# Kernel optimization log

Measured on AMD Instinct MI355X. Metric: run time of the kernel, lower is better.

## Reference

```python
import jax, jax.numpy as jnp
import numpy as np

NUM_HEADS = 4
HEAD_DIM = 16  # out_channels // num_heads = 64 // 4
IN_C = 64
OUT_C = 64


def setup_inputs() -> dict:
    key = jax.random.key(0)
    k1, k2, k3 = jax.random.split(key, 3)
    x = jax.random.normal(k1, (2, IN_C, 64, 64), dtype=jnp.float32)
    # nn.Linear(in_channels, 3*out_channels): weight (3*OUT_C, IN_C), bias (3*OUT_C,)
    s = 1.0 / np.sqrt(IN_C)
    qkv_w = jax.random.uniform(k2, (3 * OUT_C, IN_C), minval=-s, maxval=s, dtype=jnp.float32)
    qkv_b = jax.random.uniform(k3, (3 * OUT_C,), minval=-s, maxval=s, dtype=jnp.float32)
    return {"x": x, "qkv_w": qkv_w, "qkv_b": qkv_b}


def reference(x, qkv_w, qkv_b):
    B, C, H, W = x.shape
    N = H * W
    # (B,C,H,W) -> (B,N,C)
    tokens = x.reshape(B, C, N).transpose(0, 2, 1)
    qkv = tokens @ qkv_w.T + qkv_b  # (B,N,3*OUT_C)
    q, k, v = jnp.split(qkv, 3, axis=-1)
    def to_heads(t):
        return t.reshape(B, N, NUM_HEADS, HEAD_DIM).transpose(0, 2, 1, 3)  # (B,h,N,d)
    q, k, v = to_heads(q), to_heads(k), to_heads(v)
    scale = 1.0 / np.sqrt(HEAD_DIM)
    attn = jnp.einsum('bhnd,bhmd->bhnm', q, k) * scale  # (B,h,N,N)
    attn = jax.nn.softmax(attn, axis=-1)
    # dropout is identity in eval mode
    out = jnp.einsum('bhnm,bhmd->bhnd', attn, v)  # (B,h,N,d)
    out = out.transpose(0, 2, 1, 3).reshape(B, N, OUT_C)  # (B,N,outC)
    out = out.transpose(0, 2, 1).reshape(B, OUT_C, H, W)
    return out
```

## Files before the change

### kernel.cpp

```cpp
#include <hip/hip_runtime.h>
#include <hip/hip_bf16.h>


#define NTOK 4096
#define HD   16
#define BH   8
#define KT   128
#define SCH  (KT/16)
#define HALFK 2048
#define NSTAGE (HALFK/KT)

typedef __attribute__((ext_vector_type(4))) short short4v;
typedef __attribute__((ext_vector_type(4))) float float4v;
typedef __attribute__((ext_vector_type(4))) ushort ushort4v;
typedef __attribute__((ext_vector_type(2))) unsigned uint2v;

__device__ __forceinline__ ushort f2bf(float f) {
  unsigned u = __builtin_bit_cast(unsigned, f);
  u += 0x7fffu + ((u >> 16) & 1u);
  return (ushort)(u >> 16);
}

__device__ __forceinline__ float fast_exp2(float x) {
#if __has_builtin(__builtin_amdgcn_exp2f)
  return __builtin_amdgcn_exp2f(x);
#else
  return exp2f(x);
#endif
}

__device__ __forceinline__ short4v pack4_bf16(float a, float b, float c, float d) {
  __hip_bfloat162 lo = __float22bfloat162_rn(make_float2(a, b));
  __hip_bfloat162 hi = __float22bfloat162_rn(make_float2(c, d));
  unsigned ulo, uhi;
  __builtin_memcpy(&ulo, &lo, 4);
  __builtin_memcpy(&uhi, &hi, 4);
  uint2v u = { ulo, uhi };
  return __builtin_bit_cast(short4v, u);
}

#define QB_OFF 0
#define KB_OFF ((size_t)BH*NTOK*HD)
#define VT_OFF (2*(size_t)BH*NTOK*HD)

__global__ __launch_bounds__(192) void qkv_proj(
    const float* __restrict__ x, const float* __restrict__ w,
    const float* __restrict__ bias, ushort* __restrict__ wsu) {
  const int TOK = 8, TILES = 2;
  int blk = blockIdx.x;
  int b   = blk >> 8;
  int n00 = (blk & 255) * (TOK*TILES);
  int o   = threadIdx.x;

  float wr[64];
  const float4* w4 = reinterpret_cast<const float4*>(w + o*64);
  #pragma unroll
  for (int i = 0; i < 16; ++i) {
    float4 tt = w4[i];
    wr[4*i+0]=tt.x; wr[4*i+1]=tt.y; wr[4*i+2]=tt.z; wr[4*i+3]=tt.w;
  }
  float bb = bias[o];

  int part = o >> 6;
  int oo   = o & 63;
  int h    = oo >> 4;
  int dd   = oo & 15;
  int bh   = b*4 + h;
  const float QSCALE = 0.25f * 1.44269504f;

  ushort* Qt = wsu + QB_OFF;
  ushort* Kb = wsu + KB_OFF;
  ushort* Vt = wsu + VT_OFF;

  __shared__ float4 xs4[64][2];
  const float4* x4 = reinterpret_cast<const float4*>(x);

  #pragma unroll 1
  for (int tile = 0; tile < TILES; ++tile) {
    int n0 = n00 + tile*TOK;
    for (int idx = threadIdx.x; idx < 128; idx += 192) {
      int c = idx >> 1, t4 = idx & 1;
      xs4[c][t4] = x4[((size_t)b*64 + c)*(NTOK/4) + (n0 >> 2) + t4];
    }
    __syncthreads();

    #pragma unroll
    for (int t4 = 0; t4 < 2; ++t4) {
      float a[4] = {bb, bb, bb, bb};
      #pragma unroll
      for (int c = 0; c < 64; ++c) {
        float4 xv = xs4[c][t4];
        float wv = wr[c];
        a[0] = fmaf(xv.x, wv, a[0]);
        a[1] = fmaf(xv.y, wv, a[1]);
        a[2] = fmaf(xv.z, wv, a[2]);
        a[3] = fmaf(xv.w, wv, a[3]);
      }
      if (part == 0) {
        ushort4v vv = { f2bf(a[0]*QSCALE), f2bf(a[1]*QSCALE),
                        f2bf(a[2]*QSCALE), f2bf(a[3]*QSCALE) };
        *(ushort4v*)(Qt + ((size_t)bh*HD + dd)*NTOK + n0 + t4*4) = vv;
      } else if (part == 1) {
        #pragma unroll
        for (int j = 0; j < 4; ++j)
          Kb[((size_t)bh*NTOK + n0 + t4*4 + j)*HD + dd] = f2bf(a[j]);
      } else {
        ushort4v vv = { f2bf(a[0]), f2bf(a[1]), f2bf(a[2]), f2bf(a[3]) };
        *(ushort4v*)(Vt + ((size_t)bh*HD + dd)*NTOK + n0 + t4*4) = vv;
      }
    }
    __syncthreads();
  }
}

__global__ __launch_bounds__(256, 4) void attn_mfma(
    const ushort* __restrict__ wsu, float* __restrict__ out) {
  const ushort* Qt = wsu + QB_OFF;
  const ushort* Kb = wsu + KB_OFF;
  const ushort* Vt = wsu + VT_OFF;

  int bh   = blockIdx.x >> 7;
  int qblk = blockIdx.x & 127;
  int tid  = threadIdx.x;
  int wid  = tid >> 6;
  int lane = tid & 63;
  int lr   = lane & 15;
  int g4   = (lane >> 4) << 2;
  int qg   = wid & 1;
  int half = wid >> 1;
  int qbase = qblk*32 + qg*16;

  __shared__ __align__(16) char tiles[2][2][2][4096];
  __shared__ float comb[2][64][5];

  const ushort* Qh = Qt + (size_t)bh*NTOK*HD;
  const ushort* Kh = Kb + (size_t)bh*NTOK*HD + (size_t)half*HALFK*HD;
  const ushort* Vh = Vt + (size_t)bh*HD*NTOK + half*HALFK;

  short4v qf;
  qf[0] = (short)Qh[(size_t)(g4+0)*NTOK + qbase + lr];
  qf[1] = (short)Qh[(size_t)(g4+1)*NTOK + qbase + lr];
  qf[2] = (short)Qh[(size_t)(g4+2)*NTOK + qbase + lr];
  qf[3] = (short)Qh[(size_t)(g4+3)*NTOK + qbase + lr];

  size_t kgoff = (size_t)((lane >> 5)*16 + (lane & 15))*HD + ((lane >> 4) & 1)*8;
  size_t vgoff = (size_t)(lane & 15)*NTOK + (lane >> 4)*8;

  int loff = ((lane >> 5) << 8) + ((lane & 15) << 4) + (((lane >> 4) & 1) << 3);

  const short4v one4 = {(short)0x3F80, (short)0x3F80, (short)0x3F80, (short)0x3F80};

  float4v acc_e = {0.f,0.f,0.f,0.f}, acc_o = {0.f,0.f,0.f,0.f};
  float4v lac_e = {0.f,0.f,0.f,0.f}, lac_o = {0.f,0.f,0.f,0.f};

#define GLL(g, l_) __builtin_amdgcn_global_load_lds(                        \
    (const __attribute__((address_space(1))) unsigned*)(g),                 \
    (__attribute__((address_space(3))) unsigned*)(l_), 16, 0, 0)

#define STAGE(buf, s) do {                                                  \
    if (qg == 0) {                                                          \
      const ushort* gs = Kh + (size_t)(s)*(KT*HD) + kgoff;                  \
      char* lb = &tiles[buf][half][0][0];                                   \
      GLL(gs, lb); GLL(gs+512, lb+1024);                                    \
      GLL(gs+1024, lb+2048); GLL(gs+1536, lb+3072);                         \
    } else {                                                                \
      const ushort* gs = Vh + (size_t)(s)*KT + vgoff;                       \
      char* lb = &tiles[buf][half][1][0];                                   \
      GLL(gs, lb); GLL(gs+32, lb+1024);                                     \
      GLL(gs+64, lb+2048); GLL(gs+96, lb+3072);                             \
    } } while (0)

#define COMPUTE(buf) do {                                                   \
    const char* kb = &tiles[buf][half][0][0];                               \
    const char* vb = &tiles[buf][half][1][0];                               \
    __builtin_amdgcn_s_setprio(1);                                          \
    _Pragma("unroll")                                                       \
    for (int p = 0; p < SCH/2; ++p) {                                       \
      short4v kf_e = *(const short4v*)(kb + p*1024       + loff);           \
      short4v kf_o = *(const short4v*)(kb + p*1024 + 512 + loff);           \
      short4v vf_e = *(const short4v*)(vb + p*1024       + loff);           \
      short4v vf_o = *(const short4v*)(vb + p*1024 + 512 + loff);           \
      float4v zero = {0.f,0.f,0.f,0.f};                                     \
      float4v se = __builtin_amdgcn_mfma_f32_16x16x16bf16_1k(kf_e, qf, zero, 0,0,0); \
      float4v so = __builtin_amdgcn_mfma_f32_16x16x16bf16_1k(kf_o, qf, zero, 0,0,0); \
      float pe0 = fast_exp2(se[0]), pe1 = fast_exp2(se[1]);                 \
      float pe2 = fast_exp2(se[2]), pe3 = fast_exp2(se[3]);                 \
      float po0 = fast_exp2(so[0]), po1 = fast_exp2(so[1]);                 \
      float po2 = fast_exp2(so[2]), po3 = fast_exp2(so[3]);                 \
      short4v pbe = pack4_bf16(pe0, pe1, pe2, pe3);                         \
      short4v pbo = pack4_bf16(po0, po1, po2, po3);                         \
      acc_e = __builtin_amdgcn_mfma_f32_16x16x16bf16_1k(vf_e, pbe, acc_e, 0,0,0); \
      acc_o = __builtin_amdgcn_mfma_f32_16x16x16bf16_1k(vf_o, pbo, acc_o, 0,0,0); \
      lac_e = __builtin_amdgcn_mfma_f32_16x16x16bf16_1k(one4, pbe, lac_e, 0,0,0); \
      lac_o = __builtin_amdgcn_mfma_f32_16x16x16bf16_1k(one4, pbo, lac_o, 0,0,0); \
    }                                                                       \
    __builtin_amdgcn_s_setprio(0);                                          \
    } while (0)

  STAGE(0, 0);
  __syncthreads();

  #pragma unroll 1
  for (int s = 0; s < NSTAGE; s += 2) {
    if (s + 1 < NSTAGE) STAGE(1, s + 1);
    COMPUTE(0);
    __syncthreads();
    if (s + 2 < NSTAGE) STAGE(0, s + 2);
    COMPUTE(1);
    __syncthreads();
  }

  float a0 = acc_e[0] + acc_o[0];
  float a1 = acc_e[1] + acc_o[1];
  float a2 = acc_e[2] + acc_o[2];
  float a3 = acc_e[3] + acc_o[3];
  float ls = lac_e[0] + lac_o[0];

  if (half == 1) {
    comb[qg][lane][0] = a0; comb[qg][lane][1] = a1;
    comb[qg][lane][2] = a2; comb[qg][lane][3] = a3;
    comb[qg][lane][4] = ls;
  }
  __syncthreads();
  if (half == 0) {
    a0 += comb[qg][lane][0]; a1 += comb[qg][lane][1];
    a2 += comb[qg][lane][2]; a3 += comb[qg][lane][3];
    ls += comb[qg][lane][4];
    float inv = 1.0f / ls;
    int b = bh >> 2, h = bh & 3;
    float* ob = out + ((size_t)(b*64 + h*16 + g4)) * NTOK;
    ob[           qbase + lr] = a0 * inv;
    ob[  NTOK   + qbase + lr] = a1 * inv;
    ob[2*NTOK   + qbase + lr] = a2 * inv;
    ob[3*NTOK   + qbase + lr] = a3 * inv;
  }
#undef GLL
#undef STAGE
#undef COMPUTE
}

extern "C" void kernel_launch(void* const* d_in, const int* in_sizes, int n_in,
                              void* d_out, int out_size, void* d_ws, size_t ws_size,
                              hipStream_t stream) {
  const float* x    = (const float*)d_in[0];
  const float* w    = (const float*)d_in[1];
  const float* bias = (const float*)d_in[2];
  float* out  = (float*)d_out;
  ushort* wsu = (ushort*)d_ws;

  qkv_proj <<<512,  192, 0, stream>>>(x, w, bias, wsu);
  attn_mfma<<<1024, 256, 0, stream>>>(wsu, out);
}
```

Measured before the change: 43.23 us.

## Split KV into quarters with 512-thread blocks, VALU row sums, register-tiled projection

The attention kernel now splits the key range four ways (8 waves per block, smaller 64-key stages) rather than two, reusing the tile LDS for the cross-wave reduction. The row-sum MFMAs against a ones vector are replaced by scalar adds plus cross-lane shuffles. The QKV projection drops its LDS staging and computes 16 tokens per thread directly from global loads. This aims for more waves per CU and fewer MFMA instructions, at the cost of more reduction work, more barriers per key, and extra VALU adds.

```diff
diff --git a/kernel.cpp b/kernel.cpp
--- a/kernel.cpp
+++ b/kernel.cpp
@@ -5,10 +5,10 @@
 #define NTOK 4096
 #define HD   16
 #define BH   8
-#define KT   128
+#define KT   64
 #define SCH  (KT/16)
-#define HALFK 2048
-#define NSTAGE (HALFK/KT)
+#define QUART 1024
+#define NSTAGE (QUART/KT)
 
 typedef __attribute__((ext_vector_type(4))) short short4v;
 typedef __attribute__((ext_vector_type(4))) float float4v;
@@ -46,10 +46,10 @@
 __global__ __launch_bounds__(192) void qkv_proj(
     const float* __restrict__ x, const float* __restrict__ w,
     const float* __restrict__ bias, ushort* __restrict__ wsu) {
-  const int TOK = 8, TILES = 2;
+  const int TOK = 16;
   int blk = blockIdx.x;
   int b   = blk >> 8;
-  int n00 = (blk & 255) * (TOK*TILES);
+  int n0  = (blk & 255) * TOK;
   int o   = threadIdx.x;
 
   float wr[64];
@@ -61,6 +61,25 @@
   }
   float bb = bias[o];
 
+  float a[TOK];
+  #pragma unroll
+  for (int j = 0; j < TOK; ++j) a[j] = bb;
+
+  const float* xb = x + ((size_t)b*64)*NTOK + n0;
+  #pragma unroll 4
+  for (int c = 0; c < 64; ++c) {
+    const float4* xc4 = reinterpret_cast<const float4*>(xb + (size_t)c*NTOK);
+    float wv = wr[c];
+    #pragma unroll
+    for (int q4 = 0; q4 < TOK/4; ++q4) {
+      float4 xv = xc4[q4];
+      a[q4*4+0] = fmaf(xv.x, wv, a[q4*4+0]);
+      a[q4*4+1] = fmaf(xv.y, wv, a[q4*4+1]);
+      a[q4*4+2] = fmaf(xv.z, wv, a[q4*4+2]);
+      a[q4*4+3] = fmaf(xv.w, wv, a[q4*4+3]);
+    }
+  }
+
   int part = o >> 6;
   int oo   = o & 63;
   int h    = oo >> 4;
@@ -72,48 +91,28 @@
   ushort* Kb = wsu + KB_OFF;
   ushort* Vt = wsu + VT_OFF;
 
-  __shared__ float4 xs4[64][2];
-  const float4* x4 = reinterpret_cast<const float4*>(x);
-
-  #pragma unroll 1
-  for (int tile = 0; tile < TILES; ++tile) {
-    int n0 = n00 + tile*TOK;
-    for (int idx = threadIdx.x; idx < 128; idx += 192) {
-      int c = idx >> 1, t4 = idx & 1;
-      xs4[c][t4] = x4[((size_t)b*64 + c)*(NTOK/4) + (n0 >> 2) + t4];
-    }
-    __syncthreads();
-
-    #pragma unroll
-    for (int t4 = 0; t4 < 2; ++t4) {
-      float a[4] = {bb, bb, bb, bb};
-      #pragma unroll
-      for (int c = 0; c < 64; ++c) {
-        float4 xv = xs4[c][t4];
-        float wv = wr[c];
-        a[0] = fmaf(xv.x, wv, a[0]);
-        a[1] = fmaf(xv.y, wv, a[1]);
-        a[2] = fmaf(xv.z, wv, a[2]);
-        a[3] = fmaf(xv.w, wv, a[3]);
-      }
-      if (part == 0) {
-        ushort4v vv = { f2bf(a[0]*QSCALE), f2bf(a[1]*QSCALE),
-                        f2bf(a[2]*QSCALE), f2bf(a[3]*QSCALE) };
-        *(ushort4v*)(Qt + ((size_t)bh*HD + dd)*NTOK + n0 + t4*4) = vv;
-      } else if (part == 1) {
-        #pragma unroll
-        for (int j = 0; j < 4; ++j)
-          Kb[((size_t)bh*NTOK + n0 + t4*4 + j)*HD + dd] = f2bf(a[j]);
-      } else {
-        ushort4v vv = { f2bf(a[0]), f2bf(a[1]), f2bf(a[2]), f2bf(a[3]) };
-        *(ushort4v*)(Vt + ((size_t)bh*HD + dd)*NTOK + n0 + t4*4) = vv;
-      }
-    }
-    __syncthreads();
-  }
-}
-
-__global__ __launch_bounds__(256, 4) void attn_mfma(
+  if (part == 0) {
+    #pragma unroll
+    for (int q4 = 0; q4 < TOK/4; ++q4) {
+      ushort4v vv = { f2bf(a[q4*4+0]*QSCALE), f2bf(a[q4*4+1]*QSCALE),
+                      f2bf(a[q4*4+2]*QSCALE), f2bf(a[q4*4+3]*QSCALE) };
+      *(ushort4v*)(Qt + ((size_t)bh*HD + dd)*NTOK + n0 + q4*4) = vv;
+    }
+  } else if (part == 1) {
+    #pragma unroll
+    for (int j = 0; j < TOK; ++j)
+      Kb[((size_t)bh*NTOK + n0 + j)*HD + dd] = f2bf(a[j]);
+  } else {
+    #pragma unroll
+    for (int q4 = 0; q4 < TOK/4; ++q4) {
+      ushort4v vv = { f2bf(a[q4*4+0]), f2bf(a[q4*4+1]),
+                      f2bf(a[q4*4+2]), f2bf(a[q4*4+3]) };
+      *(ushort4v*)(Vt + ((size_t)bh*HD + dd)*NTOK + n0 + q4*4) = vv;
+    }
+  }
+}
+
+__global__ __launch_bounds__(512, 8) void attn_mfma(
     const ushort* __restrict__ wsu, float* __restrict__ out) {
   const ushort* Qt = wsu + QB_OFF;
   const ushort* Kb = wsu + KB_OFF;
@@ -126,16 +125,15 @@
   int lane = tid & 63;
   int lr   = lane & 15;
   int g4   = (lane >> 4) << 2;
-  int qg   = wid & 1;
-  int half = wid >> 1;
+  int qg    = wid & 1;
+  int quart = wid >> 1;
   int qbase = qblk*32 + qg*16;
 
-  __shared__ __align__(16) char tiles[2][2][2][4096];
-  __shared__ float comb[2][64][5];
+  __shared__ __align__(16) char tiles[2][4][2][2048];
 
   const ushort* Qh = Qt + (size_t)bh*NTOK*HD;
-  const ushort* Kh = Kb + (size_t)bh*NTOK*HD + (size_t)half*HALFK*HD;
-  const ushort* Vh = Vt + (size_t)bh*HD*NTOK + half*HALFK;
+  const ushort* Kh = Kb + (size_t)bh*NTOK*HD + (size_t)quart*QUART*HD;
+  const ushort* Vh = Vt + (size_t)bh*HD*NTOK + quart*QUART;
 
   short4v qf;
   qf[0] = (short)Qh[(size_t)(g4+0)*NTOK + qbase + lr];
@@ -148,10 +146,8 @@
 
   int loff = ((lane >> 5) << 8) + ((lane & 15) << 4) + (((lane >> 4) & 1) << 3);
 
-  const short4v one4 = {(short)0x3F80, (short)0x3F80, (short)0x3F80, (short)0x3F80};
-
   float4v acc_e = {0.f,0.f,0.f,0.f}, acc_o = {0.f,0.f,0.f,0.f};
-  float4v lac_e = {0.f,0.f,0.f,0.f}, lac_o = {0.f,0.f,0.f,0.f};
+  float le = 0.f, lo_ = 0.f;
 
 #define GLL(g, l_) __builtin_amdgcn_global_load_lds(                        \
     (const __attribute__((address_space(1))) unsigned*)(g),                 \
@@ -160,19 +156,17 @@
 #define STAGE(buf, s) do {                                                  \
     if (qg == 0) {                                                          \
       const ushort* gs = Kh + (size_t)(s)*(KT*HD) + kgoff;                  \
-      char* lb = &tiles[buf][half][0][0];                                   \
+      char* lb = &tiles[buf][quart][0][0];                                  \
       GLL(gs, lb); GLL(gs+512, lb+1024);                                    \
-      GLL(gs+1024, lb+2048); GLL(gs+1536, lb+3072);                         \
     } else {                                                                \
       const ushort* gs = Vh + (size_t)(s)*KT + vgoff;                       \
-      char* lb = &tiles[buf][half][1][0];                                   \
+      char* lb = &tiles[buf][quart][1][0];                                  \
       GLL(gs, lb); GLL(gs+32, lb+1024);                                     \
-      GLL(gs+64, lb+2048); GLL(gs+96, lb+3072);                             \
     } } while (0)
 
 #define COMPUTE(buf) do {                                                   \
-    const char* kb = &tiles[buf][half][0][0];                               \
-    const char* vb = &tiles[buf][half][1][0];                               \
+    const char* kb = &tiles[buf][quart][0][0];                              \
+    const char* vb = &tiles[buf][quart][1][0];                              \
     __builtin_amdgcn_s_setprio(1);                                          \
     _Pragma("unroll")                                                       \
     for (int p = 0; p < SCH/2; ++p) {                                       \
@@ -187,12 +181,12 @@
       float pe2 = fast_exp2(se[2]), pe3 = fast_exp2(se[3]);                 \
       float po0 = fast_exp2(so[0]), po1 = fast_exp2(so[1]);                 \
       float po2 = fast_exp2(so[2]), po3 = fast_exp2(so[3]);                 \
+      le  += (pe0 + pe1) + (pe2 + pe3);                                     \
+      lo_ += (po0 + po1) + (po2 + po3);                                     \
       short4v pbe = pack4_bf16(pe0, pe1, pe2, pe3);                         \
       short4v pbo = pack4_bf16(po0, po1, po2, po3);                         \
       acc_e = __builtin_amdgcn_mfma_f32_16x16x16bf16_1k(vf_e, pbe, acc_e, 0,0,0); \
       acc_o = __builtin_amdgcn_mfma_f32_16x16x16bf16_1k(vf_o, pbo, acc_o, 0,0,0); \
-      lac_e = __builtin_amdgcn_mfma_f32_16x16x16bf16_1k(one4, pbe, lac_e, 0,0,0); \
-      lac_o = __builtin_amdgcn_mfma_f32_16x16x16bf16_1k(one4, pbo, lac_o, 0,0,0); \
     }                                                                       \
     __builtin_amdgcn_s_setprio(0);                                          \
     } while (0)
@@ -210,23 +204,27 @@
     __syncthreads();
   }
 
+  float l = le + lo_;
+  l += __shfl_xor(l, 16); l += __shfl_xor(l, 32);
+
   float a0 = acc_e[0] + acc_o[0];
   float a1 = acc_e[1] + acc_o[1];
   float a2 = acc_e[2] + acc_o[2];
   float a3 = acc_e[3] + acc_o[3];
-  float ls = lac_e[0] + lac_o[0];
-
-  if (half == 1) {
-    comb[qg][lane][0] = a0; comb[qg][lane][1] = a1;
-    comb[qg][lane][2] = a2; comb[qg][lane][3] = a3;
-    comb[qg][lane][4] = ls;
+
+  float* combp = (float*)&tiles[0][0][0][0];
+  if (quart != 0) {
+    float* cp = combp + (((qg*3 + (quart-1))*64 + lane)*5);
+    cp[0] = a0; cp[1] = a1; cp[2] = a2; cp[3] = a3; cp[4] = l;
   }
   __syncthreads();
-  if (half == 0) {
-    a0 += comb[qg][lane][0]; a1 += comb[qg][lane][1];
-    a2 += comb[qg][lane][2]; a3 += comb[qg][lane][3];
-    ls += comb[qg][lane][4];
-    float inv = 1.0f / ls;
+  if (quart == 0) {
+    #pragma unroll
+    for (int p2 = 0; p2 < 3; ++p2) {
+      const float* cp = combp + (((qg*3 + p2)*64 + lane)*5);
+      a0 += cp[0]; a1 += cp[1]; a2 += cp[2]; a3 += cp[3]; l += cp[4];
+    }
+    float inv = 1.0f / l;
     int b = bh >> 2, h = bh & 3;
     float* ob = out + ((size_t)(b*64 + h*16 + g4)) * NTOK;
     ob[           qbase + lr] = a0 * inv;
@@ -249,5 +247,5 @@
   ushort* wsu = (ushort*)d_ws;
 
   qkv_proj <<<512,  192, 0, stream>>>(x, w, bias, wsu);
-  attn_mfma<<<1024, 256, 0, stream>>>(wsu, out);
-}
+  attn_mfma<<<1024, 512, 0, stream>>>(wsu, out);
+}
```

After: 46.47 us. 7.5% more time.
